# Kernel optimization log

Measured on AMD Instinct MI355X. Metric: run time of the kernel, lower is better.

The kernel has to match this reference:

```python
import jax, jax.numpy as jnp
import numpy as np

_LN_EPS = 1e-5

def _gelu(x):
    return jax.nn.gelu(x, approximate=False)

def _layernorm(x, g, b):
    mu = x.mean(-1, keepdims=True)
    var = ((x - mu) ** 2).mean(-1, keepdims=True)
    return (x - mu) * jax.lax.rsqrt(var + _LN_EPS) * g + b

def setup_inputs() -> dict:
    key = jax.random.key(0)
    ks = jax.random.split(key, 8)
    B, S, D = 4, 2048, 1024
    N_IN, N_PROC, D_R = 8192, 4096, 256
    s = 0.02
    return {
        "x": jax.random.normal(ks[0], (B, S, D), jnp.float32),
        "W1": jax.random.normal(ks[1], (2 * D_R, D), jnp.float32) * s,
        "b1": jnp.zeros((2 * D_R,), jnp.float32),
        "ln_g": jnp.ones((2 * D_R,), jnp.float32),
        "ln_b": jnp.zeros((2 * D_R,), jnp.float32),
        "W2": jax.random.normal(ks[2], (D_R, 2 * D_R), jnp.float32) * s,
        "b2": jnp.zeros((D_R,), jnp.float32),
        "neuron_keys": jax.random.normal(ks[3], (N_IN, D_R), jnp.float32) * s,
        "input_patterns": jax.random.normal(ks[4], (N_IN, D), jnp.float32) * s,
        "process_weights": jax.random.normal(ks[5], (N_PROC, N_IN), jnp.float32) * s,
        "process_outputs": jax.random.normal(ks[6], (N_PROC, D), jnp.float32) * s,
        "k_input": 4096,
        "k_process": 2048,
    }

def reference(x, W1, b1, ln_g, ln_b, W2, b2, neuron_keys, input_patterns,
              process_weights, process_outputs, k_input, k_process):
    d_routing = neuron_keys.shape[1]
    # --- Global router: sequence max-pool context -> query -> top-k input neurons
    gc = x.max(axis=1)                                   # [B, D]
    h = _layernorm(_gelu(gc @ W1.T + b1), ln_g, ln_b)    # [B, 2*d_r]
    query = h @ W2.T + b2                                # [B, d_r]
    logits = (query @ neuron_keys.T) / jnp.sqrt(jnp.asarray(d_routing, x.dtype))  # [B, N_in]
    _, input_idx = jax.lax.top_k(logits, k_input)        # [B, k_in]
    # --- Input neuron activations, gather selected ones
    input_acts = _gelu(jnp.einsum('bsd,nd->bsn', x, input_patterns))   # [B,S,N_in]
    sel_acts = jnp.take_along_axis(input_acts, input_idx[:, None, :], axis=2)  # [B,S,k_in]
    # --- Per-batch gather of process weight columns, process activations
    W_sel = jnp.take(process_weights, input_idx, axis=1)               # [N_proc,B,k_in]
    proc_acts = _gelu(jnp.einsum('bsk,pbk->bsp', sel_acts, W_sel))     # [B,S,N_proc]
    scores = proc_acts.mean(axis=1)                                    # [B,N_proc]
    _, proc_idx = jax.lax.top_k(scores, k_process)                     # [B,k_proc]
    sel_proc = jnp.take_along_axis(proc_acts, proc_idx[:, None, :], axis=2)  # [B,S,k_proc]
    out_w = process_outputs[proc_idx]                                  # [B,k_proc,D]
    return jnp.einsum('bsk,bkd->bsd', sel_proc, out_w)                 # [B,S,D]
```

## Files before the change

### kernel.cpp

```cpp
#include <hip/hip_runtime.h>
#include <cstdint>

#define B_    4
#define S_    2048
#define D_    1024
#define NIN   8192
#define NPROC 4096
#define DR    256
#define DR2   512
#define KIN   4096
#define KPROC 2048

typedef _Float16 v8h  __attribute__((ext_vector_type(8)));
typedef _Float16 v4h  __attribute__((ext_vector_type(4)));
typedef float    v4f  __attribute__((ext_vector_type(4)));
typedef float    v16f __attribute__((ext_vector_type(16)));

__device__ __forceinline__ float geluf(float v) {
    return 0.5f * v * (1.0f + erff(v * 0.70710678f));
}

__device__ __forceinline__ void cp16(void* lds, const void* g) {
    __builtin_amdgcn_global_load_lds(
        (const __attribute__((address_space(1))) unsigned int*)g,
        (__attribute__((address_space(3))) unsigned int*)lds, 16, 0, 0);
}

__global__ void k_conv_x16(const float* __restrict__ x, _Float16* __restrict__ x16, int n4) {
    int i = blockIdx.x * 256 + threadIdx.x;
    if (i < n4) {
        float4 v = ((const float4*)x)[i];
        v4h h = { (_Float16)v.x, (_Float16)v.y, (_Float16)v.z, (_Float16)v.w };
        ((v4h*)x16)[i] = h;
    }
}

__global__ void k_conv_split(const float* __restrict__ p, _Float16* __restrict__ ph,
                             _Float16* __restrict__ pl, int n) {
    int i = blockIdx.x * 256 + threadIdx.x;
    if (i < n) {
        float v = p[i];
        _Float16 h = (_Float16)v;
        ph[i] = h;
        pl[i] = (_Float16)(v - (float)h);
    }
}

__global__ void k_max1(const float* __restrict__ x, float* __restrict__ pmax) {
    int d = blockIdx.x * 256 + threadIdx.x;
    int chunk = blockIdx.y;
    int b = blockIdx.z;
    const float* base = x + ((size_t)b * S_ + chunk * 128) * D_ + d;
    float m = -3.4e38f;
    for (int s = 0; s < 128; s++) m = fmaxf(m, base[(size_t)s * D_]);
    pmax[((size_t)b * 16 + chunk) * D_ + d] = m;
}

__global__ void k_max2(const float* __restrict__ pmax, double* __restrict__ gc64) {
    int d = blockIdx.x * 256 + threadIdx.x;
    int b = blockIdx.y;
    float m = -3.4e38f;
    for (int c = 0; c < 16; c++) m = fmaxf(m, pmax[((size_t)b * 16 + c) * D_ + d]);
    gc64[(size_t)b * D_ + d] = (double)m;
}

__global__ __launch_bounds__(256) void k_router1(
    const double* __restrict__ gc64, const float* __restrict__ W1, const float* __restrict__ b1,
    double* __restrict__ hpre)
{
    int wave = threadIdx.x >> 6, lane = threadIdx.x & 63;
    int j = blockIdx.x * 4 + wave;
    int b = blockIdx.y;
    const double* g = gc64 + (size_t)b * D_;
    const float* w = W1 + (size_t)j * D_;
    double acc = 0.0;
    for (int d = lane; d < D_; d += 64) acc += g[d] * (double)w[d];
#pragma unroll
    for (int o = 32; o > 0; o >>= 1) acc += __shfl_xor(acc, o, 64);
    if (lane == 0) {
        double z = acc + (double)b1[j];
        hpre[(size_t)b * DR2 + j] = 0.5 * z * (1.0 + erf(z * 0.7071067811865475244));
    }
}

__global__ __launch_bounds__(512) void k_router2(
    const double* __restrict__ hpre, const float* __restrict__ lng, const float* __restrict__ lnb,
    const float* __restrict__ W2, const float* __restrict__ b2, double* __restrict__ qs)
{
    __shared__ double sh[DR2];
    __shared__ double red[DR2];
    int b = blockIdx.x, j = threadIdx.x;
    double ge = hpre[(size_t)b * DR2 + j];
    sh[j] = ge; red[j] = ge;
    __syncthreads();
    for (int s = 256; s > 0; s >>= 1) { if (j < s) red[j] += red[j + s]; __syncthreads(); }
    double mu = red[0] / 512.0;
    __syncthreads();
    double dv = ge - mu;
    red[j] = dv * dv;
    __syncthreads();
    for (int s = 256; s > 0; s >>= 1) { if (j < s) red[j] += red[j + s]; __syncthreads(); }
    double rs = 1.0 / sqrt(red[0] / 512.0 + 1e-5);
    __syncthreads();
    sh[j] = dv * rs * (double)lng[j] + (double)lnb[j];
    __syncthreads();
    if (j < DR) {
        double q = (double)b2[j];
        const float* w2r = W2 + (size_t)j * DR2;
        for (int t = 0; t < DR2; t++) q += sh[t] * (double)w2r[t];
        qs[(size_t)b * DR + j] = q;
    }
}

__global__ __launch_bounds__(256) void k_router3(
    const double* __restrict__ qs, const float* __restrict__ keys, double* __restrict__ logits)
{
    int wave = threadIdx.x >> 6, lane = threadIdx.x & 63;
    int n = blockIdx.x * 4 + wave;
    int b = blockIdx.y;
    const double* q = qs + (size_t)b * DR;
    const float* kr = keys + (size_t)n * DR;
    double acc = 0.0;
#pragma unroll
    for (int t = 0; t < 4; t++) {
        int d = lane + t * 64;
        acc += q[d] * (double)kr[d];
    }
#pragma unroll
    for (int o = 32; o > 0; o >>= 1) acc += __shfl_xor(acc, o, 64);
    if (lane == 0) logits[(size_t)b * NIN + n] = acc * 0.0625;
}

template<int N, int K>
__global__ __launch_bounds__(1024) void k_topk(const double* __restrict__ vals, int* __restrict__ outIdx) {
    __shared__ unsigned long long keys[N];
    int b = blockIdx.x, tid = threadIdx.x;
    for (int i = tid; i < N; i += 1024) {
        float v = (float)vals[(size_t)b * N + i];
        unsigned int u = __float_as_uint(v);
        u = (u & 0x80000000u) ? ~u : (u | 0x80000000u);
        keys[i] = ((unsigned long long)u << 32) | (unsigned int)(~i);
    }
    __syncthreads();
    for (int k = 2; k <= N; k <<= 1)
        for (int j = k >> 1; j > 0; j >>= 1) {
            for (int i = tid; i < N; i += 1024) {
                int l = i ^ j;
                if (l > i) {
                    unsigned long long a = keys[i], c = keys[l];
                    bool up = ((i & k) == 0);
                    if ((a < c) == up) { keys[i] = c; keys[l] = a; }
                }
            }
            __syncthreads();
        }
    for (int i = tid; i < K; i += 1024)
        outIdx[(size_t)b * K + i] = (int)(~(unsigned int)keys[i]);
}

__device__ __forceinline__ void dev_gatherW(const float* __restrict__ pw, const int* __restrict__ iidx,
                                            _Float16* __restrict__ Wh, _Float16* __restrict__ Wl,
                                            int p, int b, size_t bstride) {
    const float* row = pw + (size_t)p * NIN;
    const int* ix = iidx + (size_t)b * KIN;
    _Float16* wh = Wh + bstride + (size_t)p * KIN;
    _Float16* wl = Wl + bstride + (size_t)p * KIN;
    for (int j = threadIdx.x; j < KIN; j += 256) {
        float w = row[ix[j]];
        _Float16 h = (_Float16)w;
        wh[j] = h;
        wl[j] = (_Float16)(w - (float)h);
    }
}

__global__ void k_gatherSP(const _Float16* __restrict__ acts16, const int* __restrict__ pidx,
                           _Float16* __restrict__ sp) {
    int s = blockIdx.x, b = blockIdx.y;
    const _Float16* arow = acts16 + ((size_t)b * S_ + s) * NPROC;
    _Float16* orow = sp + ((size_t)b * S_ + s) * KPROC;
    const int* pi = pidx + (size_t)b * KPROC;
    for (int k = threadIdx.x; k < KPROC; k += 256) orow[k] = arow[pi[k]];
}

__global__ void k_gatherWoT(const _Float16* __restrict__ pout16, const int* __restrict__ pidx,
                            _Float16* __restrict__ woT) {
    __shared__ _Float16 t[64][65];
    int k0 = blockIdx.x * 64, d0 = blockIdx.y * 64, b = blockIdx.z;
    const int* pi = pidx + (size_t)b * KPROC;
    for (int i = threadIdx.x; i < 4096; i += 256) {
        int kk = i >> 6, dd = i & 63;
        t[kk][dd] = pout16[(size_t)pi[k0 + kk] * D_ + d0 + dd];
    }
    __syncthreads();
    for (int i = threadIdx.x; i < 4096; i += 256) {
        int dd = i >> 6, kk = i & 63;
        woT[((size_t)b * D_ + d0 + dd) * KPROC + k0 + kk] = t[kk][dd];
    }
}


__device__ __forceinline__ void dev_gemmD(
    const _Float16* __restrict__ x16, const _Float16* __restrict__ ph, const _Float16* __restrict__ pl,
    const int* __restrict__ iidx, _Float16* __restrict__ a16,
    _Float16* tA, _Float16* tBh, _Float16* tBl, int bx, int by, int b)
{
    const int m0 = bx * 128, n0 = by * 128;
    const int tid = threadIdx.x, lane = tid & 63;
    const int wave = tid >> 6, wrow = wave >> 1, wcol = wave & 1;
    const int srow = tid >> 2, spart = tid & 3;
    const int spe = spart ^ ((srow >> 1) & 3);

    const _Float16* as0 = x16 + ((size_t)b * S_ + m0 + srow) * D_ + spe * 8;
    const _Float16* as1 = as0 + (size_t)64 * D_;
    int r0 = iidx[(size_t)b * KIN + n0 + srow];
    int r1 = iidx[(size_t)b * KIN + n0 + srow + 64];
    const _Float16* bh0 = ph + (size_t)r0 * D_ + spe * 8;
    const _Float16* bh1 = ph + (size_t)r1 * D_ + spe * 8;
    const _Float16* bl0 = pl + (size_t)r0 * D_ + spe * 8;
    const _Float16* bl1 = pl + (size_t)r1 * D_ + spe * 8;

    v16f acc[2][2];
#pragma unroll
    for (int i = 0; i < 2; i++)
#pragma unroll
        for (int j = 0; j < 2; j++) acc[i][j] = (v16f)(0.0f);

    const int lrow = lane & 31, lhi = lane >> 5;
    const int swz = (lane >> 1) & 3;
    const int abase = (wrow * 64 + lrow) * 32;
    const int bbase = (wcol * 64 + lrow) * 32;

    for (int kt = 0; kt < D_; kt += 32) {
        __syncthreads();
        cp16(&tA[tid * 8], as0 + kt);
        cp16(&tA[2048 + tid * 8], as1 + kt);
        cp16(&tBh[tid * 8], bh0 + kt);
        cp16(&tBh[2048 + tid * 8], bh1 + kt);
        cp16(&tBl[tid * 8], bl0 + kt);
        cp16(&tBl[2048 + tid * 8], bl1 + kt);
        asm volatile("s_waitcnt vmcnt(0)" ::: "memory");
        __syncthreads();
        v8h af[2][2], fh[2][2], fl[2][2];
#pragma unroll
        for (int kw = 0; kw < 2; kw++) {
            const int ch = ((kw * 2 + lhi) ^ swz) * 8;
#pragma unroll
            for (int mi = 0; mi < 2; mi++) af[mi][kw] = *(const v8h*)&tA[abase + mi * 1024 + ch];
#pragma unroll
            for (int nj = 0; nj < 2; nj++) {
                fh[nj][kw] = *(const v8h*)&tBh[bbase + nj * 1024 + ch];
                fl[nj][kw] = *(const v8h*)&tBl[bbase + nj * 1024 + ch];
            }
        }
#pragma unroll
        for (int kw = 0; kw < 2; kw++)
#pragma unroll
            for (int mi = 0; mi < 2; mi++)
#pragma unroll
                for (int nj = 0; nj < 2; nj++) {
                    acc[mi][nj] = __builtin_amdgcn_mfma_f32_32x32x16_f16(af[mi][kw], fh[nj][kw], acc[mi][nj], 0, 0, 0);
                    acc[mi][nj] = __builtin_amdgcn_mfma_f32_32x32x16_f16(af[mi][kw], fl[nj][kw], acc[mi][nj], 0, 0, 0);
                }
    }
#pragma unroll
    for (int mi = 0; mi < 2; mi++)
#pragma unroll
        for (int nj = 0; nj < 2; nj++)
#pragma unroll
            for (int r = 0; r < 16; r++) {
                int row = (r & 3) + 8 * (r >> 2) + 4 * lhi;
                float gv = geluf(acc[mi][nj][r]);
                a16[((size_t)b * S_ + m0 + wrow * 64 + mi * 32 + row) * (size_t)KIN
                    + n0 + wcol * 64 + nj * 32 + lrow] = (_Float16)gv;
            }
}

__global__ __launch_bounds__(256, 3) void k_gemmD(
    const _Float16* __restrict__ x16, const _Float16* __restrict__ ph, const _Float16* __restrict__ pl,
    const int* __restrict__ iidx, _Float16* __restrict__ a16)
{
    __shared__ _Float16 tA[4096], tBh[4096], tBl[4096];
    dev_gemmD(x16, ph, pl, iidx, a16, tA, tBh, tBl, blockIdx.x, blockIdx.y, blockIdx.z);
}

__global__ __launch_bounds__(256, 3) void k_fusedDW(
    const _Float16* __restrict__ x16, const _Float16* __restrict__ ph, const _Float16* __restrict__ pl,
    const int* __restrict__ iidx, _Float16* __restrict__ a16,
    const float* __restrict__ pw, _Float16* __restrict__ Wh, _Float16* __restrict__ Wl, size_t wstride)
{
    __shared__ _Float16 tA[4096], tBh[4096], tBl[4096];
    if (blockIdx.z >= 4) {
        int idx = (blockIdx.z - 4) * 512 + blockIdx.y * 16 + blockIdx.x;
        int p = idx >> 2, b = idx & 3;
        dev_gatherW(pw, iidx, Wh, Wl, p, b, (size_t)b * wstride);
        return;
    }
    dev_gemmD(x16, ph, pl, iidx, a16, tA, tBh, tBl, blockIdx.x, blockIdx.y, blockIdx.z);
}

__global__ void k_gatherW(const float* __restrict__ pw, const int* __restrict__ iidx,
                          _Float16* __restrict__ Wh, _Float16* __restrict__ Wl,
                          int b_base, size_t wstride) {
    dev_gatherW(pw, iidx, Wh, Wl, blockIdx.x, b_base + blockIdx.y, (size_t)blockIdx.y * wstride);
}

__global__ __launch_bounds__(256, 3) void k_gemmE(
    const _Float16* __restrict__ a16, const _Float16* __restrict__ Wh, const _Float16* __restrict__ Wl,
    _Float16* __restrict__ acts16, double* __restrict__ scores, int b_base, size_t wstride)
{
    const int b = b_base + blockIdx.z;
    const int m0 = blockIdx.x * 128, n0 = blockIdx.y * 128;
    __shared__ _Float16 tA[4096], tBh[4096], tBl[4096];
    const int tid = threadIdx.x, lane = tid & 63;
    const int wave = tid >> 6, wrow = wave >> 1, wcol = wave & 1;
    const int srow = tid >> 2, spart = tid & 3;
    const int spe = spart ^ ((srow >> 1) & 3);

    const _Float16* as0 = a16 + ((size_t)b * S_ + m0 + srow) * (size_t)KIN + spe * 8;
    const _Float16* as1 = as0 + (size_t)64 * KIN;
    const _Float16* whB = Wh + (size_t)blockIdx.z * wstride;
    const _Float16* wlB = Wl + (size_t)blockIdx.z * wstride;
    const _Float16* bh0 = whB + (size_t)(n0 + srow) * KIN + spe * 8;
    const _Float16* bh1 = bh0 + (size_t)64 * KIN;
    const _Float16* bl0 = wlB + (size_t)(n0 + srow) * KIN + spe * 8;
    const _Float16* bl1 = bl0 + (size_t)64 * KIN;

    v16f acc[2][2];
#pragma unroll
    for (int i = 0; i < 2; i++)
#pragma unroll
        for (int j = 0; j < 2; j++) acc[i][j] = (v16f)(0.0f);

    const int lrow = lane & 31, lhi = lane >> 5;
    const int swz = (lane >> 1) & 3;
    const int abase = (wrow * 64 + lrow) * 32;
    const int bbase = (wcol * 64 + lrow) * 32;

    for (int kt = 0; kt < KIN; kt += 32) {
        __syncthreads();
        cp16(&tA[tid * 8], as0 + kt);
        cp16(&tA[2048 + tid * 8], as1 + kt);
        cp16(&tBh[tid * 8], bh0 + kt);
        cp16(&tBh[2048 + tid * 8], bh1 + kt);
        cp16(&tBl[tid * 8], bl0 + kt);
        cp16(&tBl[2048 + tid * 8], bl1 + kt);
        asm volatile("s_waitcnt vmcnt(0)" ::: "memory");
        __syncthreads();
        v8h af[2][2], fh[2][2], fl[2][2];
#pragma unroll
        for (int kw = 0; kw < 2; kw++) {
            const int ch = ((kw * 2 + lhi) ^ swz) * 8;
#pragma unroll
            for (int mi = 0; mi < 2; mi++) af[mi][kw] = *(const v8h*)&tA[abase + mi * 1024 + ch];
#pragma unroll
            for (int nj = 0; nj < 2; nj++) {
                fh[nj][kw] = *(const v8h*)&tBh[bbase + nj * 1024 + ch];
                fl[nj][kw] = *(const v8h*)&tBl[bbase + nj * 1024 + ch];
            }
        }
#pragma unroll
        for (int kw = 0; kw < 2; kw++)
#pragma unroll
            for (int mi = 0; mi < 2; mi++)
#pragma unroll
                for (int nj = 0; nj < 2; nj++) {
                    acc[mi][nj] = __builtin_amdgcn_mfma_f32_32x32x16_f16(af[mi][kw], fh[nj][kw], acc[mi][nj], 0, 0, 0);
                    acc[mi][nj] = __builtin_amdgcn_mfma_f32_32x32x16_f16(af[mi][kw], fl[nj][kw], acc[mi][nj], 0, 0, 0);
                }
    }
    float psum[2] = {0.f, 0.f};
#pragma unroll
    for (int mi = 0; mi < 2; mi++)
#pragma unroll
        for (int nj = 0; nj < 2; nj++)
#pragma unroll
            for (int r = 0; r < 16; r++) {
                int row = (r & 3) + 8 * (r >> 2) + 4 * lhi;
                float gv = geluf(acc[mi][nj][r]);
                acts16[((size_t)b * S_ + m0 + wrow * 64 + mi * 32 + row) * (size_t)NPROC
                       + n0 + wcol * 64 + nj * 32 + lrow] = (_Float16)gv;
                psum[nj] += gv;
            }
#pragma unroll
    for (int nj = 0; nj < 2; nj++) {
        float s = psum[nj];
        s += __shfl_xor(s, 32, 64);
        if (lhi == 0)
            atomicAdd(&scores[(size_t)b * NPROC + n0 + wcol * 64 + nj * 32 + lrow], (double)s);
    }
}

__global__ __launch_bounds__(256, 3) void k_gemmF(
    const _Float16* __restrict__ sp, const _Float16* __restrict__ woT, float* __restrict__ out)
{
    const int b = blockIdx.z;
    const int m0 = blockIdx.x * 128, n0 = blockIdx.y * 128;
    __shared__ _Float16 tA[4096], tB[4096];
    const int tid = threadIdx.x, lane = tid & 63;
    const int wave = tid >> 6, wrow = wave >> 1, wcol = wave & 1;
    const int srow = tid >> 2, spart = tid & 3;
    const int spe = spart ^ ((srow >> 1) & 3);

    const _Float16* as0 = sp + ((size_t)b * S_ + m0 + srow) * (size_t)KPROC + spe * 8;
    const _Float16* as1 = as0 + (size_t)64 * KPROC;
    const _Float16* bs0 = woT + ((size_t)b * D_ + n0 + srow) * (size_t)KPROC + spe * 8;
    const _Float16* bs1 = bs0 + (size_t)64 * KPROC;

    v16f acc[2][2];
#pragma unroll
    for (int i = 0; i < 2; i++)
#pragma unroll
        for (int j = 0; j < 2; j++) acc[i][j] = (v16f)(0.0f);

    const int lrow = lane & 31, lhi = lane >> 5;
    const int swz = (lane >> 1) & 3;
    const int abase = (wrow * 64 + lrow) * 32;
    const int bbase = (wcol * 64 + lrow) * 32;

    for (int kt = 0; kt < KPROC; kt += 32) {
        __syncthreads();
        cp16(&tA[tid * 8], as0 + kt);
        cp16(&tA[2048 + tid * 8], as1 + kt);
        cp16(&tB[tid * 8], bs0 + kt);
        cp16(&tB[2048 + tid * 8], bs1 + kt);
        asm volatile("s_waitcnt vmcnt(0)" ::: "memory");
        __syncthreads();
        v8h af[2][2], bf[2][2];
#pragma unroll
        for (int kw = 0; kw < 2; kw++) {
            const int ch = ((kw * 2 + lhi) ^ swz) * 8;
#pragma unroll
            for (int mi = 0; mi < 2; mi++) af[mi][kw] = *(const v8h*)&tA[abase + mi * 1024 + ch];
#pragma unroll
            for (int nj = 0; nj < 2; nj++) bf[nj][kw] = *(const v8h*)&tB[bbase + nj * 1024 + ch];
        }
#pragma unroll
        for (int kw = 0; kw < 2; kw++)
#pragma unroll
            for (int mi = 0; mi < 2; mi++)
#pragma unroll
                for (int nj = 0; nj < 2; nj++)
                    acc[mi][nj] = __builtin_amdgcn_mfma_f32_32x32x16_f16(af[mi][kw], bf[nj][kw], acc[mi][nj], 0, 0, 0);
    }
#pragma unroll
    for (int mi = 0; mi < 2; mi++)
#pragma unroll
        for (int nj = 0; nj < 2; nj++)
#pragma unroll
            for (int r = 0; r < 16; r++) {
                int row = (r & 3) + 8 * (r >> 2) + 4 * lhi;
                out[((size_t)b * S_ + m0 + wrow * 64 + mi * 32 + row) * (size_t)D_
                    + n0 + wcol * 64 + nj * 32 + lrow] = acc[mi][nj][r];
            }
}

extern "C" void kernel_launch(void* const* d_in, const int* in_sizes, int n_in,
                              void* d_out, int out_size, void* d_ws, size_t ws_size,
                              hipStream_t stream) {
    const float* x    = (const float*)d_in[0];
    const float* W1   = (const float*)d_in[1];
    const float* b1   = (const float*)d_in[2];
    const float* lng  = (const float*)d_in[3];
    const float* lnb  = (const float*)d_in[4];
    const float* W2   = (const float*)d_in[5];
    const float* b2   = (const float*)d_in[6];
    const float* keys = (const float*)d_in[7];
    const float* patt = (const float*)d_in[8];
    const float* pw   = (const float*)d_in[9];
    const float* pout = (const float*)d_in[10];
    (void)in_sizes; (void)n_in; (void)out_size;

    char* w = (char*)d_ws;
    size_t off = 0;
    auto alloc = [&](size_t bytes) -> void* {
        void* p = w + off;
        off += (bytes + 255) & ~(size_t)255;
        return p;
    };
    double* gc64   = (double*)alloc((size_t)B_ * D_ * 8);
    float*  pmax   = (float*) alloc((size_t)B_ * 16 * D_ * 4);
    double* logits = (double*)alloc((size_t)B_ * NIN * 8);
    double* scores = (double*)alloc((size_t)B_ * NPROC * 8);
    double* hpre   = (double*)alloc((size_t)B_ * DR2 * 8);
    double* qs     = (double*)alloc((size_t)B_ * DR * 8);
    int*    iidx   = (int*)   alloc((size_t)B_ * KIN * 4);
    int*    pidx   = (int*)   alloc((size_t)B_ * KPROC * 4);
    _Float16* a16    = (_Float16*)alloc((size_t)B_ * S_ * KIN * 2);
    _Float16* acts16 = (_Float16*)alloc((size_t)B_ * S_ * NPROC * 2);
    _Float16* pout16 = (_Float16*)alloc((size_t)NPROC * D_ * 2);
    char* u1 = (char*)alloc((size_t)67108864);
    _Float16* x16 = (_Float16*)u1;
    _Float16* ph  = (_Float16*)(u1 + 16777216);
    _Float16* pl  = (_Float16*)(u1 + 33554432);
    _Float16* WhT = (_Float16*)u1;
    _Float16* WlT = (_Float16*)(u1 + 33554432);
    _Float16* sp  = (_Float16*)u1;
    _Float16* woT = (_Float16*)(u1 + 33554432);

    const size_t WSTRIDE = (size_t)NPROC * KIN;
    size_t off_before_fat = off;
    _Float16* WhA = (_Float16*)alloc((size_t)B_ * WSTRIDE * 2);
    _Float16* WlA = (_Float16*)alloc((size_t)B_ * WSTRIDE * 2);
    bool fat = (off <= ws_size);
    if (!fat) off = off_before_fat;

    hipMemsetAsync(scores, 0, (size_t)B_ * NPROC * 8, stream);

    k_conv_x16 <<<dim3((B_ * S_ * D_ / 4 + 255) / 256), 256, 0, stream>>>(x, x16, B_ * S_ * D_ / 4);
    k_conv_split<<<dim3((NIN * D_ + 255) / 256), 256, 0, stream>>>(patt, ph, pl, NIN * D_);
    k_conv_x16 <<<dim3((NPROC * D_ / 4 + 255) / 256), 256, 0, stream>>>(pout, pout16, NPROC * D_ / 4);

    k_max1<<<dim3(4, 16, 4), 256, 0, stream>>>(x, pmax);
    k_max2<<<dim3(4, 4), 256, 0, stream>>>(pmax, gc64);
    k_router1<<<dim3(128, 4), 256, 0, stream>>>(gc64, W1, b1, hpre);
    k_router2<<<dim3(4), 512, 0, stream>>>(hpre, lng, lnb, W2, b2, qs);
    k_router3<<<dim3(2048, 4), 256, 0, stream>>>(qs, keys, logits);
    k_topk<NIN, KIN><<<dim3(4), 1024, 0, stream>>>(logits, iidx);

    if (fat) {
        k_fusedDW<<<dim3(16, 32, 36), 256, 0, stream>>>(x16, ph, pl, iidx, a16, pw, WhA, WlA, WSTRIDE);
        k_gemmE<<<dim3(16, 32, 4), 256, 0, stream>>>(a16, WhA, WlA, acts16, scores, 0, WSTRIDE);
    } else {
        k_gemmD<<<dim3(16, 32, 4), 256, 0, stream>>>(x16, ph, pl, iidx, a16);
        for (int b = 0; b < 4; b++) {
            k_gatherW<<<dim3(NPROC, 1), 256, 0, stream>>>(pw, iidx, WhT, WlT, b, 0);
            k_gemmE<<<dim3(16, 32, 1), 256, 0, stream>>>(a16, WhT, WlT, acts16, scores, b, 0);
        }
    }

    k_topk<NPROC, KPROC><<<dim3(4), 1024, 0, stream>>>(scores, pidx);
    k_gatherSP<<<dim3(S_, 4), 256, 0, stream>>>(acts16, pidx, sp);
    k_gatherWoT<<<dim3(KPROC / 64, D_ / 64, 4), 256, 0, stream>>>(pout16, pidx, woT);
    k_gemmF<<<dim3(16, 8, 4), 256, 0, stream>>>(sp, woT, (float*)d_out);
}
```

Measured before the change: 1.572 ms.

## Double-buffer LDS tiles in GEMM kernels to overlap loads with MFMA

```diff
diff --git a/kernel.cpp b/kernel.cpp
--- a/kernel.cpp
+++ b/kernel.cpp
@@ -230,26 +230,38 @@
     const int abase = (wrow * 64 + lrow) * 32;
     const int bbase = (wcol * 64 + lrow) * 32;
 
+    cp16(&tA[tid * 8], as0);
+    cp16(&tA[2048 + tid * 8], as1);
+    cp16(&tBh[tid * 8], bh0);
+    cp16(&tBh[2048 + tid * 8], bh1);
+    cp16(&tBl[tid * 8], bl0);
+    cp16(&tBl[2048 + tid * 8], bl1);
+    asm volatile("s_waitcnt vmcnt(0)" ::: "memory");
+    __syncthreads();
+
     for (int kt = 0; kt < D_; kt += 32) {
-        __syncthreads();
-        cp16(&tA[tid * 8], as0 + kt);
-        cp16(&tA[2048 + tid * 8], as1 + kt);
-        cp16(&tBh[tid * 8], bh0 + kt);
-        cp16(&tBh[2048 + tid * 8], bh1 + kt);
-        cp16(&tBl[tid * 8], bl0 + kt);
-        cp16(&tBl[2048 + tid * 8], bl1 + kt);
-        asm volatile("s_waitcnt vmcnt(0)" ::: "memory");
-        __syncthreads();
+        const int cur = (kt >> 5) & 1;
+        const int o = cur * 4096;
+        if (kt + 32 < D_) {
+            const int on = (cur ^ 1) * 4096;
+            const int kn = kt + 32;
+            cp16(&tA[on + tid * 8], as0 + kn);
+            cp16(&tA[on + 2048 + tid * 8], as1 + kn);
+            cp16(&tBh[on + tid * 8], bh0 + kn);
+            cp16(&tBh[on + 2048 + tid * 8], bh1 + kn);
+            cp16(&tBl[on + tid * 8], bl0 + kn);
+            cp16(&tBl[on + 2048 + tid * 8], bl1 + kn);
+        }
         v8h af[2][2], fh[2][2], fl[2][2];
 #pragma unroll
         for (int kw = 0; kw < 2; kw++) {
             const int ch = ((kw * 2 + lhi) ^ swz) * 8;
 #pragma unroll
-            for (int mi = 0; mi < 2; mi++) af[mi][kw] = *(const v8h*)&tA[abase + mi * 1024 + ch];
+            for (int mi = 0; mi < 2; mi++) af[mi][kw] = *(const v8h*)&tA[o + abase + mi * 1024 + ch];
 #pragma unroll
             for (int nj = 0; nj < 2; nj++) {
-                fh[nj][kw] = *(const v8h*)&tBh[bbase + nj * 1024 + ch];
-                fl[nj][kw] = *(const v8h*)&tBl[bbase + nj * 1024 + ch];
+                fh[nj][kw] = *(const v8h*)&tBh[o + bbase + nj * 1024 + ch];
+                fl[nj][kw] = *(const v8h*)&tBl[o + bbase + nj * 1024 + ch];
             }
         }
 #pragma unroll
@@ -261,6 +273,8 @@
                     acc[mi][nj] = __builtin_amdgcn_mfma_f32_32x32x16_f16(af[mi][kw], fh[nj][kw], acc[mi][nj], 0, 0, 0);
                     acc[mi][nj] = __builtin_amdgcn_mfma_f32_32x32x16_f16(af[mi][kw], fl[nj][kw], acc[mi][nj], 0, 0, 0);
                 }
+        asm volatile("s_waitcnt vmcnt(0)" ::: "memory");
+        __syncthreads();
     }
 #pragma unroll
     for (int mi = 0; mi < 2; mi++)
@@ -279,7 +293,7 @@
     const _Float16* __restrict__ x16, const _Float16* __restrict__ ph, const _Float16* __restrict__ pl,
     const int* __restrict__ iidx, _Float16* __restrict__ a16)
 {
-    __shared__ _Float16 tA[4096], tBh[4096], tBl[4096];
+    __shared__ _Float16 tA[8192], tBh[8192], tBl[8192];
     dev_gemmD(x16, ph, pl, iidx, a16, tA, tBh, tBl, blockIdx.x, blockIdx.y, blockIdx.z);
 }
 
@@ -288,7 +302,7 @@
     const int* __restrict__ iidx, _Float16* __restrict__ a16,
     const float* __restrict__ pw, _Float16* __restrict__ Wh, _Float16* __restrict__ Wl, size_t wstride)
 {
-    __shared__ _Float16 tA[4096], tBh[4096], tBl[4096];
+    __shared__ _Float16 tA[8192], tBh[8192], tBl[8192];
     if (blockIdx.z >= 4) {
         int idx = (blockIdx.z - 4) * 512 + blockIdx.y * 16 + blockIdx.x;
         int p = idx >> 2, b = idx & 3;
@@ -310,7 +324,7 @@
 {
     const int b = b_base + blockIdx.z;
     const int m0 = blockIdx.x * 128, n0 = blockIdx.y * 128;
-    __shared__ _Float16 tA[4096], tBh[4096], tBl[4096];
+    __shared__ _Float16 tA[8192], tBh[8192], tBl[8192];
     const int tid = threadIdx.x, lane = tid & 63;
     const int wave = tid >> 6, wrow = wave >> 1, wcol = wave & 1;
     const int srow = tid >> 2, spart = tid & 3;
@@ -336,26 +350,38 @@
     const int abase = (wrow * 64 + lrow) * 32;
     const int bbase = (wcol * 64 + lrow) * 32;
 
+    cp16(&tA[tid * 8], as0);
+    cp16(&tA[2048 + tid * 8], as1);
+    cp16(&tBh[tid * 8], bh0);
+    cp16(&tBh[2048 + tid * 8], bh1);
+    cp16(&tBl[tid * 8], bl0);
+    cp16(&tBl[2048 + tid * 8], bl1);
+    asm volatile("s_waitcnt vmcnt(0)" ::: "memory");
+    __syncthreads();
+
     for (int kt = 0; kt < KIN; kt += 32) {
-        __syncthreads();
-        cp16(&tA[tid * 8], as0 + kt);
-        cp16(&tA[2048 + tid * 8], as1 + kt);
-        cp16(&tBh[tid * 8], bh0 + kt);
-        cp16(&tBh[2048 + tid * 8], bh1 + kt);
-        cp16(&tBl[tid * 8], bl0 + kt);
-        cp16(&tBl[2048 + tid * 8], bl1 + kt);
-        asm volatile("s_waitcnt vmcnt(0)" ::: "memory");
-        __syncthreads();
+        const int cur = (kt >> 5) & 1;
+        const int o = cur * 4096;
+        if (kt + 32 < KIN) {
+            const int on = (cur ^ 1) * 4096;
+            const int kn = kt + 32;
+            cp16(&tA[on + tid * 8], as0 + kn);
+            cp16(&tA[on + 2048 + tid * 8], as1 + kn);
+            cp16(&tBh[on + tid * 8], bh0 + kn);
+            cp16(&tBh[on + 2048 + tid * 8], bh1 + kn);
+            cp16(&tBl[on + tid * 8], bl0 + kn);
+            cp16(&tBl[on + 2048 + tid * 8], bl1 + kn);
+        }
         v8h af[2][2], fh[2][2], fl[2][2];
 #pragma unroll
         for (int kw = 0; kw < 2; kw++) {
             const int ch = ((kw * 2 + lhi) ^ swz) * 8;
 #pragma unroll
-            for (int mi = 0; mi < 2; mi++) af[mi][kw] = *(const v8h*)&tA[abase + mi * 1024 + ch];
+            for (int mi = 0; mi < 2; mi++) af[mi][kw] = *(const v8h*)&tA[o + abase + mi * 1024 + ch];
 #pragma unroll
             for (int nj = 0; nj < 2; nj++) {
-                fh[nj][kw] = *(const v8h*)&tBh[bbase + nj * 1024 + ch];
-                fl[nj][kw] = *(const v8h*)&tBl[bbase + nj * 1024 + ch];
+                fh[nj][kw] = *(const v8h*)&tBh[o + bbase + nj * 1024 + ch];
+                fl[nj][kw] = *(const v8h*)&tBl[o + bbase + nj * 1024 + ch];
             }
         }
 #pragma unroll
@@ -367,6 +393,8 @@
                     acc[mi][nj] = __builtin_amdgcn_mfma_f32_32x32x16_f16(af[mi][kw], fh[nj][kw], acc[mi][nj], 0, 0, 0);
                     acc[mi][nj] = __builtin_amdgcn_mfma_f32_32x32x16_f16(af[mi][kw], fl[nj][kw], acc[mi][nj], 0, 0, 0);
                 }
+        asm volatile("s_waitcnt vmcnt(0)" ::: "memory");
+        __syncthreads();
     }
     float psum[2] = {0.f, 0.f};
 #pragma unroll
@@ -395,7 +423,7 @@
 {
     const int b = blockIdx.z;
     const int m0 = blockIdx.x * 128, n0 = blockIdx.y * 128;
-    __shared__ _Float16 tA[4096], tB[4096];
+    __shared__ _Float16 tA[8192], tB[8192];
     const int tid = threadIdx.x, lane = tid & 63;
     const int wave = tid >> 6, wrow = wave >> 1, wcol = wave & 1;
     const int srow = tid >> 2, spart = tid & 3;
@@ -417,30 +445,42 @@
     const int abase = (wrow * 64 + lrow) * 32;
     const int bbase = (wcol * 64 + lrow) * 32;
 
+    cp16(&tA[tid * 8], as0);
+    cp16(&tA[2048 + tid * 8], as1);
+    cp16(&tB[tid * 8], bs0);
+    cp16(&tB[2048 + tid * 8], bs1);
+    asm volatile("s_waitcnt vmcnt(0)" ::: "memory");
+    __syncthreads();
+
     for (int kt = 0; kt < KPROC; kt += 32) {
-        __syncthreads();
-        cp16(&tA[tid * 8], as0 + kt);
-        cp16(&tA[2048 + tid * 8], as1 + kt);
-        cp16(&tB[tid * 8], bs0 + kt);
-        cp16(&tB[2048 + tid * 8], bs1 + kt);
+        const int cur = (kt >> 5) & 1;
+        const int o = cur * 4096;
+        if (kt + 32 < KPROC) {
+            const int on = (cur ^ 1) * 4096;
+            const int kn = kt + 32;
+            cp16(&tA[on + tid * 8], as0 + kn);
+            cp16(&tA[on + 2048 + tid * 8], as1 + kn);
+            cp16(&tB[on + tid * 8], bs0 + kn);
+            cp16(&tB[on + 2048 + tid * 8], bs1 + kn);
+        }
+        v8h af[2][2], bf[2][2];
+#pragma unroll
+        for (int kw = 0; kw < 2; kw++) {
+            const int ch = ((kw * 2 + lhi) ^ swz) * 8;
+#pragma unroll
+            for (int mi = 0; mi < 2; mi++) af[mi][kw] = *(const v8h*)&tA[o + abase + mi * 1024 + ch];
+#pragma unroll
+            for (int nj = 0; nj < 2; nj++) bf[nj][kw] = *(const v8h*)&tB[o + bbase + nj * 1024 + ch];
+        }
+#pragma unroll
+        for (int kw = 0; kw < 2; kw++)
+#pragma unroll
+            for (int mi = 0; mi < 2; mi++)
+#pragma unroll
+                for (int nj = 0; nj < 2; nj++)
+                    acc[mi][nj] = __builtin_amdgcn_mfma_f32_32x32x16_f16(af[mi][kw], bf[nj][kw], acc[mi][nj], 0, 0, 0);
         asm volatile("s_waitcnt vmcnt(0)" ::: "memory");
         __syncthreads();
-        v8h af[2][2], bf[2][2];
-#pragma unroll
-        for (int kw = 0; kw < 2; kw++) {
-            const int ch = ((kw * 2 + lhi) ^ swz) * 8;
-#pragma unroll
-            for (int mi = 0; mi < 2; mi++) af[mi][kw] = *(const v8h*)&tA[abase + mi * 1024 + ch];
-#pragma unroll
-            for (int nj = 0; nj < 2; nj++) bf[nj][kw] = *(const v8h*)&tB[bbase + nj * 1024 + ch];
-        }
-#pragma unroll
-        for (int kw = 0; kw < 2; kw++)
-#pragma unroll
-            for (int mi = 0; mi < 2; mi++)
-#pragma unroll
-                for (int nj = 0; nj < 2; nj++)
-                    acc[mi][nj] = __builtin_amdgcn_mfma_f32_32x32x16_f16(af[mi][kw], bf[nj][kw], acc[mi][nj], 0, 0, 0);
     }
 #pragma unroll
     for (int mi = 0; mi < 2; mi++)
```

Result: no change. 1.574 ms (+0.1%).
